# Kernel optimization log

Hardware: AMD Instinct MI355X
Metric: run time of the kernel (lower is better)

## Reference

```python
import jax, jax.numpy as jnp
from jax import lax
import numpy as np

B, S, D, H, L, DFF = 64, 512, 512, 8, 6, 2048
CLIP_C = 10.0
EPS = 1e-5


def setup_inputs() -> dict:
    key = jax.random.key(0)
    ks = jax.random.split(key, 16)
    sc = 0.02
    inp = {
        "x": jax.random.normal(ks[0], (B, S, D), jnp.float32),
        "mask": jnp.zeros((B, S, S), jnp.float32),
        # stacked per-layer params [L, ...]; Linear stored as (out, in) like torch
        "qkv_w": jax.random.normal(ks[1], (L, 3 * D, D), jnp.float32) * sc,
        "qkv_b": jnp.zeros((L, 3 * D), jnp.float32),
        "ln1_g": jnp.ones((L, D), jnp.float32),
        "ln1_b": jnp.zeros((L, D), jnp.float32),
        "kv_w": jax.random.normal(ks[2], (L, 2 * D, D), jnp.float32) * sc,
        "kv_b": jnp.zeros((L, 2 * D), jnp.float32),
        "ln2_g": jnp.ones((L, D), jnp.float32),
        "ln2_b": jnp.zeros((L, D), jnp.float32),
        "w1": jax.random.normal(ks[3], (L, DFF, D), jnp.float32) * sc,
        "b1": jnp.zeros((L, DFF), jnp.float32),
        "w2": jax.random.normal(ks[4], (L, D, DFF), jnp.float32) * sc,
        "b2": jnp.zeros((L, D), jnp.float32),
        "ln3_g": jnp.ones((L, D), jnp.float32),
        "ln3_b": jnp.zeros((L, D), jnp.float32),
    }
    return inp


def _ln(v, g, b):
    m = v.mean(-1, keepdims=True)
    var = ((v - m) ** 2).mean(-1, keepdims=True)
    return (v - m) * lax.rsqrt(var + EPS) * g + b


def _mha(q, k, v, mask, clip_c):
    # faithful to custom_multi_head_attn: bmm -> /sqrt(hd) -> [c*tanh] -> +mask -> softmax -> bmm
    b, sq, d = q.shape
    sk = k.shape[1]
    hd = d // H
    qh = q.reshape(b, sq, H, hd)
    kh = k.reshape(b, sk, H, hd)
    vh = v.reshape(b, sk, H, hd)
    s = jnp.einsum('bqhd,bkhd->bhqk', qh, kh) * (1.0 / float(hd) ** 0.5)
    if clip_c is not None:
        s = clip_c * jnp.tanh(s)
    if mask is not None:
        s = s + mask[:, None]  # repeat over heads
    a = jax.nn.softmax(s, axis=-1)
    return jnp.einsum('bhqk,bkhd->bqhd', a, vh).reshape(b, sq, d)


def reference(x, mask, qkv_w, qkv_b, ln1_g, ln1_b, kv_w, kv_b, ln2_g, ln2_b,
              w1, b1, w2, b2, ln3_g, ln3_b):
    def step(h, p):
        (qw, qb, g1, be1, kw, kb, g2, be2, fw1, fb1, fw2, fb2, g3, be3) = p
        # self-attention block (no FFN, no mask, no clip; note: NO out-projection,
        # matching the original which never applies out_proj_weight)
        qkv = h @ qw.T + qb
        q, k, v = jnp.split(qkv, 3, axis=-1)
        x1 = _ln(h + _mha(q, k, v, None, None), g1, be1)
        # cross-attention block: query = sa output (no q_proj), kv from original h
        kv_ = h @ kw.T + kb
        k2, v2 = jnp.split(kv_, 2, axis=-1)
        y = _ln(x1 + _mha(x1, k2, v2, mask, CLIP_C), g2, be2)
        # FFN + residual + norm (post-norm)
        ff = jax.nn.relu(y @ fw1.T + fb1) @ fw2.T + fb2
        return _ln(y + ff, g3, be3), None

    params = (qkv_w, qkv_b, ln1_g, ln1_b, kv_w, kv_b, ln2_g, ln2_b,
              w1, b1, w2, b2, ln3_g, ln3_b)
    out, _ = lax.scan(step, x, params)
    return out
```

## Files before the change

### kernel.cpp

```cpp
#include <hip/hip_runtime.h>


typedef __bf16 bf16_t;
typedef __bf16 bf16x8 __attribute__((ext_vector_type(8)));
typedef __bf16 bf16x4 __attribute__((ext_vector_type(4)));
typedef float  f32x4  __attribute__((ext_vector_type(4)));

#define NB   64
#define NS   512
#define ND   512
#define NH   8
#define NHD  64
#define NL   6
#define NDFF 2048
#define NM   (NB * NS)

__device__ __forceinline__ void gld_lds16(const void* gsrc, void* lds) {
  __builtin_amdgcn_global_load_lds((__attribute__((address_space(1))) void*)gsrc,
                                   (__attribute__((address_space(3))) void*)lds,
                                   16, 0, 0);
}

template<int N> __device__ __forceinline__ void vm_wait() {
  if constexpr (N == 0)      asm volatile("s_waitcnt vmcnt(0)" ::: "memory");
  else if constexpr (N == 3) asm volatile("s_waitcnt vmcnt(3)" ::: "memory");
}
__device__ __forceinline__ void lgkm0() {
  asm volatile("s_waitcnt lgkmcnt(0)" ::: "memory");
}

__global__ __launch_bounds__(256) void cvt_f32_bf16(const float* __restrict__ in,
                                                    bf16_t* __restrict__ out,
                                                    long n) {
  long i = ((long)blockIdx.x * 256 + threadIdx.x) * 8;
  const long stride = (long)gridDim.x * 256 * 8;
  for (; i < n; i += stride) {
    f32x4 a = *(const f32x4*)(in + i);
    f32x4 b = *(const f32x4*)(in + i + 4);
    bf16x8 o;
#pragma unroll
    for (int j = 0; j < 4; ++j) { o[j] = (bf16_t)a[j]; o[j + 4] = (bf16_t)b[j]; }
    *(bf16x8*)(out + i) = o;
  }
}

template<bool RELU, bool BIAS_ROW>
__global__ __launch_bounds__(512, 4) void gemm128n(const bf16_t* __restrict__ Ap,
                                                   const bf16_t* __restrict__ Wp,
                                                   const float* __restrict__ bias,
                                                   bf16_t* __restrict__ Cout,
                                                   int Nn, int Kk) {
  __shared__ __attribute__((aligned(16))) bf16_t As[2][256 * 32];
  __shared__ __attribute__((aligned(16))) bf16_t Bs[2][128 * 32];
  const int tid = threadIdx.x;
  const int l   = tid & 63;
  const int w   = tid >> 6;
  const int wr  = w >> 2;
  const int wc  = w & 3;
  const int l15 = l & 15, lg = l >> 4;

  const int nn   = Nn >> 7;
  const int nwg  = gridDim.x;
  const int flat = blockIdx.x;
  const int wgid = (nwg & 7) ? flat : (flat & 7) * (nwg >> 3) + (flat >> 3);
  const int m0 = (wgid / nn) * 256;
  const int n0 = (wgid % nn) * 128;

  const int srow = tid >> 2;
  const int sg   = (tid & 3) ^ (srow & 3);

  auto stA = [&](int bf_, int p, int kc) {
    gld_lds16(Ap + (size_t)(m0 + p * 128 + srow) * Kk + kc + sg * 8,
              &As[bf_][(p * 128 + w * 16) * 32]);
  };
  auto stB = [&](int bf_, int kc) {
    gld_lds16(Wp + (size_t)(n0 + srow) * Kk + kc + sg * 8,
              &Bs[bf_][(w * 16) * 32]);
  };
  auto stage = [&](int kt, int bf_) {
    const int kc = kt * 32;
    stA(bf_, 0, kc); stA(bf_, 1, kc); stB(bf_, kc);
  };
  auto ldA = [&](int bf_, int mi) -> bf16x8 {
    const int row = wr * 128 + mi * 16 + l15;
    return *(const bf16x8*)&As[bf_][row * 32 + ((lg ^ (row & 3)) * 8)];
  };
  auto ldB = [&](int bf_, int ni) -> bf16x8 {
    const int row = wc * 32 + ni * 16 + l15;
    return *(const bf16x8*)&Bs[bf_][row * 32 + ((lg ^ (row & 3)) * 8)];
  };

  f32x4 acc[8][2];
#pragma unroll
  for (int i = 0; i < 8; ++i) { acc[i][0] = (f32x4){0,0,0,0}; acc[i][1] = (f32x4){0,0,0,0}; }

  const int KT = Kk >> 5;
  stage(0, 0);
  stage(1, 1);

  for (int kt = 0; kt < KT; ++kt) {
    const int buf = kt & 1;
    if (kt + 1 < KT) vm_wait<3>(); else vm_wait<0>();
    __builtin_amdgcn_s_barrier();

    bf16x8 bf0 = ldB(buf, 0), bf1 = ldB(buf, 1);
    __builtin_amdgcn_s_setprio(1);
#pragma unroll
    for (int mi = 0; mi < 8; ++mi) {
      bf16x8 af = ldA(buf, mi);
      acc[mi][0] = __builtin_amdgcn_mfma_f32_16x16x32_bf16(af, bf0, acc[mi][0], 0, 0, 0);
      acc[mi][1] = __builtin_amdgcn_mfma_f32_16x16x32_bf16(af, bf1, acc[mi][1], 0, 0, 0);
    }
    __builtin_amdgcn_s_setprio(0);

    lgkm0();
    __builtin_amdgcn_s_barrier();
    if (kt + 2 < KT) stage(kt + 2, buf);
  }

#pragma unroll
  for (int mf = 0; mf < 8; ++mf)
#pragma unroll
    for (int ni = 0; ni < 2; ++ni) {
      const int col = n0 + wc * 32 + ni * 16 + l15;
      const float bc = BIAS_ROW ? 0.f : bias[col];
#pragma unroll
      for (int r = 0; r < 4; ++r) {
        const int rowi = m0 + wr * 128 + mf * 16 + lg * 4 + r;
        float v = acc[mf][ni][r] + (BIAS_ROW ? bias[rowi] : bc);
        if (RELU) v = fmaxf(v, 0.f);
        Cout[(size_t)rowi * Nn + col] = (bf16_t)v;
      }
    }
}

template<int CROSS>
__global__ __launch_bounds__(256, 2) void attn3(const bf16_t* __restrict__ Q,
                                                const bf16_t* __restrict__ K,
                                                const bf16_t* __restrict__ Vt,
                                                const float* __restrict__ maskp,
                                                bf16_t* __restrict__ O,
                                                int qstride, int kstride, int vstride) {
  __shared__ __attribute__((aligned(16))) bf16_t k_s[2][128 * 64];
  __shared__ __attribute__((aligned(16))) bf16_t v_s[2][64 * 128];
  __shared__ __attribute__((aligned(16))) bf16_t p_s[64 * 128];

  const int tid = threadIdx.x;
  const int l   = tid & 63;
  const int w   = tid >> 6;
  const int bid = blockIdx.x;
  const int h   = bid & 7;
  const int qt  = (bid >> 3) & 7;
  const int b   = bid >> 6;
  const int h64 = h * NHD;
  const int l15 = l & 15, lg = l >> 4;

  const int qglob = qt * 64 + w * 16 + l15;

  auto stageK = [&](int kt, int buf) {
#pragma unroll
    for (int i = 0; i < 4; ++i) {
      const int r  = (w * 4 + i) * 8 + (l >> 3);
      const int c8 = (l & 7) ^ (r & 7);
      gld_lds16(K + (size_t)(b * NS + kt * 128 + r) * kstride + h64 + c8 * 8,
                &k_s[buf][(w * 4 + i) * 512]);
    }
  };
  auto stageV = [&](int kt, int buf) {
#pragma unroll
    for (int i = 0; i < 4; ++i) {
      const int d = w * 16 + i * 4 + (l >> 4);
      const int g = (l & 15) ^ (d & 15);
      gld_lds16(Vt + (size_t)(h64 + d) * vstride + b * NS + kt * 128 + g * 8,
                &v_s[buf][(w * 16 + i * 4) * 128]);
    }
  };

  stageK(0, 0); stageV(0, 0);

  bf16x8 qf[2];
#pragma unroll
  for (int c = 0; c < 2; ++c)
    qf[c] = *(const bf16x8*)(Q + (size_t)(b * NS + qglob) * qstride + h64 + c * 32 + lg * 8);

  f32x4 mk[2][8];
  if (CROSS) {
#pragma unroll
    for (int nt = 0; nt < 8; ++nt)
      mk[0][nt] = *(const f32x4*)(maskp + (size_t)(b * NS + qglob) * NS + nt * 16 + lg * 4);
  }

  float m_run = -3e38f, l_run = 0.f;
  const f32x4 zz = {0.f, 0.f, 0.f, 0.f};
  f32x4 oacc[4] = {zz, zz, zz, zz};

#pragma unroll
  for (int kt = 0; kt < 4; ++kt) {
    const int buf = kt & 1;
    __syncthreads();
    if (kt < 3) {
      stageK(kt + 1, buf ^ 1);
      stageV(kt + 1, buf ^ 1);
      if (CROSS) {
#pragma unroll
        for (int nt = 0; nt < 8; ++nt)
          mk[(kt + 1) & 1][nt] = *(const f32x4*)(maskp + (size_t)(b * NS + qglob) * NS
                                                 + (kt + 1) * 128 + nt * 16 + lg * 4);
      }
    }

    f32x4 s[8];
    __builtin_amdgcn_s_setprio(1);
#pragma unroll
    for (int nt = 0; nt < 8; ++nt) {
      const int row = nt * 16 + l15;
      bf16x8 ka0 = *(const bf16x8*)((const char*)k_s[buf] + row * 128 + ((lg ^ (row & 7)) * 16));
      bf16x8 ka1 = *(const bf16x8*)((const char*)k_s[buf] + row * 128 + (((4 + lg) ^ (row & 7)) * 16));
      f32x4 z = zz;
      z = __builtin_amdgcn_mfma_f32_16x16x32_bf16(ka0, qf[0], z, 0, 0, 0);
      z = __builtin_amdgcn_mfma_f32_16x16x32_bf16(ka1, qf[1], z, 0, 0, 0);
      s[nt] = z;
    }
    __builtin_amdgcn_s_setprio(0);

    float tmax = -3e38f;
#pragma unroll
    for (int nt = 0; nt < 8; ++nt) {
      f32x4 v = s[nt] * 0.125f;
      if (CROSS) {
#pragma unroll
        for (int r = 0; r < 4; ++r) {
          const float e2 = __expf(2.f * v[r]);
          v[r] = 10.f - 20.f * __builtin_amdgcn_rcpf(e2 + 1.f) + mk[buf][nt][r];
        }
      }
      s[nt] = v;
#pragma unroll
      for (int r = 0; r < 4; ++r) tmax = fmaxf(tmax, v[r]);
    }
    tmax = fmaxf(tmax, __shfl_xor(tmax, 16, 64));
    tmax = fmaxf(tmax, __shfl_xor(tmax, 32, 64));
    const float m_new = fmaxf(m_run, tmax);
    const float f = __expf(m_run - m_new);
    float fq[4];
#pragma unroll
    for (int r = 0; r < 4; ++r) fq[r] = __shfl(f, lg * 4 + r, 64);
#pragma unroll
    for (int dt = 0; dt < 4; ++dt)
#pragma unroll
      for (int r = 0; r < 4; ++r) oacc[dt][r] *= fq[r];

    float ts = 0.f;
#pragma unroll
    for (int nt = 0; nt < 8; ++nt) {
      f32x4 v = s[nt];
#pragma unroll
      for (int r = 0; r < 4; ++r) { const float e = __expf(v[r] - m_new); ts += e; v[r] = e; }
      s[nt] = v;
    }
    l_run = l_run * f + ts;
    m_run = m_new;

    const int prow = w * 16 + l15;
#pragma unroll
    for (int nt = 0; nt < 8; ++nt) {
      bf16x4 pk;
#pragma unroll
      for (int r = 0; r < 4; ++r) pk[r] = (bf16_t)s[nt][r];
      const int gran = (nt * 2 + (lg >> 1)) ^ (prow & 15);
      *(bf16x4*)((char*)p_s + prow * 256 + gran * 16 + (lg & 1) * 8) = pk;
    }

    __builtin_amdgcn_s_setprio(1);
#pragma unroll
    for (int ks = 0; ks < 4; ++ks) {
      const int ag = (ks * 4 + lg) ^ (prow & 15);
      bf16x8 pa = *(const bf16x8*)((const char*)p_s + prow * 256 + ag * 16);
#pragma unroll
      for (int dt = 0; dt < 4; ++dt) {
        const int vrow = dt * 16 + l15;
        const int vg   = (ks * 4 + lg) ^ (vrow & 15);
        bf16x8 vb = *(const bf16x8*)((const char*)v_s[buf] + vrow * 256 + vg * 16);
        oacc[dt] = __builtin_amdgcn_mfma_f32_16x16x32_bf16(pa, vb, oacc[dt], 0, 0, 0);
      }
    }
    __builtin_amdgcn_s_setprio(0);
  }

  l_run += __shfl_xor(l_run, 16, 64);
  l_run += __shfl_xor(l_run, 32, 64);
  const float inv = 1.f / l_run;
  float invq[4];
#pragma unroll
  for (int r = 0; r < 4; ++r) invq[r] = __shfl(inv, lg * 4 + r, 64);
#pragma unroll
  for (int dt = 0; dt < 4; ++dt)
#pragma unroll
    for (int r = 0; r < 4; ++r) {
      const size_t row = (size_t)(b * NS + qt * 64 + w * 16 + lg * 4 + r);
      O[row * ND + h64 + dt * 16 + l15] = (bf16_t)(oacc[dt][r] * invq[r]);
    }
}

template<bool A16, bool W32>
__global__ __launch_bounds__(256) void add_ln2(const void* __restrict__ Xav,
                                               const bf16_t* __restrict__ Xb,
                                               const float* __restrict__ gw,
                                               const float* __restrict__ bw,
                                               float* __restrict__ o32,
                                               bf16_t* __restrict__ o16) {
  const int l = threadIdx.x & 63;
  const size_t row  = (size_t)blockIdx.x * 4 + (threadIdx.x >> 6);
  const size_t base = row * ND + l * 8;
  f32x4 a0, a1;
  if (A16) {
    bf16x8 t = *(const bf16x8*)((const bf16_t*)Xav + base);
#pragma unroll
    for (int i = 0; i < 4; ++i) { a0[i] = (float)t[i]; a1[i] = (float)t[i + 4]; }
  } else {
    a0 = *(const f32x4*)((const float*)Xav + base);
    a1 = *(const f32x4*)((const float*)Xav + base + 4);
  }
  bf16x8 tb = *(const bf16x8*)(Xb + base);
  f32x4 b0, b1;
#pragma unroll
  for (int i = 0; i < 4; ++i) { b0[i] = (float)tb[i]; b1[i] = (float)tb[i + 4]; }
  f32x4 v0 = a0 + b0, v1 = a1 + b1;
  float s = v0[0] + v0[1] + v0[2] + v0[3] + v1[0] + v1[1] + v1[2] + v1[3];
#pragma unroll
  for (int off = 1; off < 64; off <<= 1) s += __shfl_xor(s, off, 64);
  const float mean = s * (1.f / ND);
  f32x4 d0 = v0 - mean, d1 = v1 - mean;
  float q = d0[0]*d0[0] + d0[1]*d0[1] + d0[2]*d0[2] + d0[3]*d0[3]
          + d1[0]*d1[0] + d1[1]*d1[1] + d1[2]*d1[2] + d1[3]*d1[3];
#pragma unroll
  for (int off = 1; off < 64; off <<= 1) q += __shfl_xor(q, off, 64);
  const float rstd = rsqrtf(q * (1.f / ND) + 1e-5f);
  const f32x4 g0 = *(const f32x4*)(gw + l * 8), g1 = *(const f32x4*)(gw + l * 8 + 4);
  const f32x4 h0 = *(const f32x4*)(bw + l * 8), h1 = *(const f32x4*)(bw + l * 8 + 4);
  f32x4 r0 = d0 * rstd * g0 + h0;
  f32x4 r1 = d1 * rstd * g1 + h1;
  if (W32) {
    *(f32x4*)(o32 + base)     = r0;
    *(f32x4*)(o32 + base + 4) = r1;
  } else {
    bf16x8 o;
#pragma unroll
    for (int i = 0; i < 4; ++i) { o[i] = (bf16_t)r0[i]; o[i + 4] = (bf16_t)r1[i]; }
    *(bf16x8*)(o16 + base) = o;
  }
}

extern "C" void kernel_launch(void* const* d_in, const int* in_sizes, int n_in,
                              void* d_out, int out_size, void* d_ws, size_t ws_size,
                              hipStream_t stream) {
  (void)in_sizes; (void)n_in; (void)out_size;
  const float* x     = (const float*)d_in[0];
  const float* maskp = (const float*)d_in[1];
  const float* qkvw  = (const float*)d_in[2];
  const float* qkvb  = (const float*)d_in[3];
  const float* ln1g  = (const float*)d_in[4];
  const float* ln1b  = (const float*)d_in[5];
  const float* kvw   = (const float*)d_in[6];
  const float* kvb   = (const float*)d_in[7];
  const float* ln2g  = (const float*)d_in[8];
  const float* ln2b  = (const float*)d_in[9];
  const float* w1p   = (const float*)d_in[10];
  const float* b1p   = (const float*)d_in[11];
  const float* w2p   = (const float*)d_in[12];
  const float* b2p   = (const float*)d_in[13];
  const float* ln3g  = (const float*)d_in[14];
  const float* ln3b  = (const float*)d_in[15];
  float* out = (float*)d_out;

  const size_t WALL = 40894464, WLYR = 6815744, H16B = 33554432;
  struct Tier { int R; bool allw; };
  const Tier tiers[6] = {{32768, true}, {16384, true}, {8192, true},
                         {4096, true}, {2048, false}, {1024, false}};
  int R = 0; bool allw = false;
  for (int t = 0; t < 6; ++t) {
    size_t need = (tiers[t].allw ? WALL : WLYR) + H16B +
                  (size_t)tiers[t].R * 7168 + 16384;
    if (ws_size >= need) { R = tiers[t].R; allw = tiers[t].allw; break; }
  }
  if (R == 0) return;
  const int nchunks = NM / R;
  const int CB = R / NS;
  const int MT = R / 256;

  char* p = (char*)d_ws;
  auto alloc = [&](size_t bytes) { char* r = p; p += (bytes + 255) & ~(size_t)255; return r; };
  bf16_t* WQ = (bf16_t*)alloc((allw ? NL : 1) * (size_t)1536 * ND * 2);
  bf16_t* WK = (bf16_t*)alloc((allw ? NL : 1) * (size_t)1024 * ND * 2);
  bf16_t* W1 = (bf16_t*)alloc((allw ? NL : 1) * (size_t)NDFF * ND * 2);
  bf16_t* W2 = (bf16_t*)alloc((allw ? NL : 1) * (size_t)ND * NDFF * 2);
  bf16_t* h16  = (bf16_t*)alloc((size_t)NM * ND * 2);
  bf16_t* big  = (bf16_t*)alloc((size_t)R * NDFF * 2);
  bf16_t* t16  = (bf16_t*)alloc((size_t)R * ND * 2);
  bf16_t* x116 = (bf16_t*)alloc((size_t)R * ND * 2);
  bf16_t* y16  = (bf16_t*)alloc((size_t)R * ND * 2);

  auto cvt = [&](const float* src, bf16_t* dst, long n) {
    int blocks = (int)((n / 8 + 255) / 256); if (blocks > 8192) blocks = 8192;
    hipLaunchKernelGGL(cvt_f32_bf16, dim3(blocks), dim3(256), 0, stream, src, dst, n);
  };

  cvt(x, h16, (long)NM * ND);
  if (allw) {
    cvt(qkvw, WQ, (long)NL * 1536 * ND);
    cvt(kvw,  WK, (long)NL * 1024 * ND);
    cvt(w1p,  W1, (long)NL * NDFF * ND);
    cvt(w2p,  W2, (long)NL * ND * NDFF);
  }

  for (int l = 0; l < NL; ++l) {
    const bf16_t *wq_l, *wk_l, *w1_l, *w2_l;
    if (allw) {
      wq_l = WQ + (size_t)l * 1536 * ND;
      wk_l = WK + (size_t)l * 1024 * ND;
      w1_l = W1 + (size_t)l * NDFF * ND;
      w2_l = W2 + (size_t)l * ND * NDFF;
    } else {
      cvt(qkvw + (size_t)l * 1536 * ND, WQ, (long)1536 * ND);
      cvt(kvw  + (size_t)l * 1024 * ND, WK, (long)1024 * ND);
      cvt(w1p  + (size_t)l * NDFF * ND, W1, (long)NDFF * ND);
      cvt(w2p  + (size_t)l * ND * NDFF, W2, (long)ND * NDFF);
      wq_l = WQ; wk_l = WK; w1_l = W1; w2_l = W2;
    }

    for (int c = 0; c < nchunks; ++c) {
      const size_t r0 = (size_t)c * R;
      bf16_t*       h16c  = h16 + r0 * ND;
      const float*  maskc = maskp + r0 * NS;
      bf16_t* vtS = big + (size_t)R * 1024;
      bf16_t* vtC = big + (size_t)R * 512;

      hipLaunchKernelGGL(HIP_KERNEL_NAME(gemm128n<false, false>), dim3(MT * 8), dim3(512), 0, stream,
                         h16c, wq_l, qkvb + l * 1536, big, 1024, 512);
      hipLaunchKernelGGL(HIP_KERNEL_NAME(gemm128n<false, true>), dim3(2 * (R / 128)), dim3(512), 0, stream,
                         wq_l + (size_t)1024 * 512, h16c, qkvb + l * 1536 + 1024, vtS, R, 512);
      hipLaunchKernelGGL(HIP_KERNEL_NAME(attn3<0>), dim3(CB * 64), dim3(256), 0, stream,
                         big, big + 512, vtS, (const float*)nullptr, t16, 1024, 1024, R);
      if (l == 0)
        hipLaunchKernelGGL(HIP_KERNEL_NAME(add_ln2<false, false>), dim3(R / 4), dim3(256), 0, stream,
                           (const void*)(x + r0 * ND), t16, ln1g, ln1b, (float*)nullptr, x116);
      else
        hipLaunchKernelGGL(HIP_KERNEL_NAME(add_ln2<true, false>), dim3(R / 4), dim3(256), 0, stream,
                           (const void*)h16c, t16, ln1g + l * ND, ln1b + l * ND, (float*)nullptr, x116);
      hipLaunchKernelGGL(HIP_KERNEL_NAME(gemm128n<false, false>), dim3(MT * 4), dim3(512), 0, stream,
                         h16c, wk_l, kvb + l * 1024, big, 512, 512);
      hipLaunchKernelGGL(HIP_KERNEL_NAME(gemm128n<false, true>), dim3(2 * (R / 128)), dim3(512), 0, stream,
                         wk_l + (size_t)512 * 512, h16c, kvb + l * 1024 + 512, vtC, R, 512);
      hipLaunchKernelGGL(HIP_KERNEL_NAME(attn3<1>), dim3(CB * 64), dim3(256), 0, stream,
                         x116, big, vtC, maskc, t16, 512, 512, R);
      hipLaunchKernelGGL(HIP_KERNEL_NAME(add_ln2<true, false>), dim3(R / 4), dim3(256), 0, stream,
                         (const void*)x116, t16, ln2g + l * ND, ln2b + l * ND, (float*)nullptr, y16);
      hipLaunchKernelGGL(HIP_KERNEL_NAME(gemm128n<true, false>), dim3(MT * 16), dim3(512), 0, stream,
                         y16, w1_l, b1p + l * NDFF, big, 2048, 512);
      hipLaunchKernelGGL(HIP_KERNEL_NAME(gemm128n<false, false>), dim3(MT * 4), dim3(512), 0, stream,
                         big, w2_l, b2p + l * ND, t16, 512, 2048);
      if (l < NL - 1)
        hipLaunchKernelGGL(HIP_KERNEL_NAME(add_ln2<true, false>), dim3(R / 4), dim3(256), 0, stream,
                           (const void*)y16, t16, ln3g + l * ND, ln3b + l * ND, (float*)nullptr, h16c);
      else
        hipLaunchKernelGGL(HIP_KERNEL_NAME(add_ln2<true, true>), dim3(R / 4), dim3(256), 0, stream,
                           (const void*)y16, t16, ln3g + l * ND, ln3b + l * ND, out + r0 * ND, (bf16_t*)nullptr);
    }
  }
}
```

Measured before the change: 4.062 ms.

## Retile GEMM to 128x256 squarer warp tiles, shrink attention KV tile, add bf16 mask

The GEMM changes from 256x128 tiles with 8x2 MFMA fragments per warp to 128x256 tiles with 4x4 fragments per warp. This raises fragment reuse per LDS load and changes grid sizes. The attention kernel now uses 64-key tiles instead of 128, halving LDS use so it can run at occupancy 4 instead of 2. When workspace allows, the mask is converted once to bf16 to halve its read traffic in cross-attention, at the cost of an extra conversion pass and a larger workspace.

```diff
diff --git a/kernel.cpp b/kernel.cpp
--- a/kernel.cpp
+++ b/kernel.cpp
@@ -45,13 +45,13 @@
 }
 
 template<bool RELU, bool BIAS_ROW>
-__global__ __launch_bounds__(512, 4) void gemm128n(const bf16_t* __restrict__ Ap,
-                                                   const bf16_t* __restrict__ Wp,
-                                                   const float* __restrict__ bias,
-                                                   bf16_t* __restrict__ Cout,
-                                                   int Nn, int Kk) {
-  __shared__ __attribute__((aligned(16))) bf16_t As[2][256 * 32];
-  __shared__ __attribute__((aligned(16))) bf16_t Bs[2][128 * 32];
+__global__ __launch_bounds__(512, 4) void gemm64(const bf16_t* __restrict__ Ap,
+                                                 const bf16_t* __restrict__ Wp,
+                                                 const float* __restrict__ bias,
+                                                 bf16_t* __restrict__ Cout,
+                                                 int Nn, int Kk) {
+  __shared__ __attribute__((aligned(16))) bf16_t As[2][128 * 32];
+  __shared__ __attribute__((aligned(16))) bf16_t Bs[2][256 * 32];
   const int tid = threadIdx.x;
   const int l   = tid & 63;
   const int w   = tid >> 6;
@@ -59,40 +59,42 @@
   const int wc  = w & 3;
   const int l15 = l & 15, lg = l >> 4;
 
-  const int nn   = Nn >> 7;
+  const int nn   = Nn >> 8;
   const int nwg  = gridDim.x;
   const int flat = blockIdx.x;
   const int wgid = (nwg & 7) ? flat : (flat & 7) * (nwg >> 3) + (flat >> 3);
-  const int m0 = (wgid / nn) * 256;
-  const int n0 = (wgid % nn) * 128;
+  const int m0 = (wgid / nn) * 128;
+  const int n0 = (wgid % nn) * 256;
 
   const int srow = tid >> 2;
   const int sg   = (tid & 3) ^ (srow & 3);
 
-  auto stA = [&](int bf_, int p, int kc) {
-    gld_lds16(Ap + (size_t)(m0 + p * 128 + srow) * Kk + kc + sg * 8,
-              &As[bf_][(p * 128 + w * 16) * 32]);
-  };
-  auto stB = [&](int bf_, int kc) {
-    gld_lds16(Wp + (size_t)(n0 + srow) * Kk + kc + sg * 8,
-              &Bs[bf_][(w * 16) * 32]);
+  auto stA = [&](int bf_, int kc) {
+    gld_lds16(Ap + (size_t)(m0 + srow) * Kk + kc + sg * 8,
+              &As[bf_][(w * 16) * 32]);
+  };
+  auto stB = [&](int bf_, int p, int kc) {
+    gld_lds16(Wp + (size_t)(n0 + p * 128 + srow) * Kk + kc + sg * 8,
+              &Bs[bf_][(p * 128 + w * 16) * 32]);
   };
   auto stage = [&](int kt, int bf_) {
     const int kc = kt * 32;
-    stA(bf_, 0, kc); stA(bf_, 1, kc); stB(bf_, kc);
+    stA(bf_, kc); stB(bf_, 0, kc); stB(bf_, 1, kc);
   };
   auto ldA = [&](int bf_, int mi) -> bf16x8 {
-    const int row = wr * 128 + mi * 16 + l15;
+    const int row = wr * 64 + mi * 16 + l15;
     return *(const bf16x8*)&As[bf_][row * 32 + ((lg ^ (row & 3)) * 8)];
   };
   auto ldB = [&](int bf_, int ni) -> bf16x8 {
-    const int row = wc * 32 + ni * 16 + l15;
+    const int row = wc * 64 + ni * 16 + l15;
     return *(const bf16x8*)&Bs[bf_][row * 32 + ((lg ^ (row & 3)) * 8)];
   };
 
-  f32x4 acc[8][2];
-#pragma unroll
-  for (int i = 0; i < 8; ++i) { acc[i][0] = (f32x4){0,0,0,0}; acc[i][1] = (f32x4){0,0,0,0}; }
+  f32x4 acc[4][4];
+#pragma unroll
+  for (int i = 0; i < 4; ++i)
+#pragma unroll
+    for (int j = 0; j < 4; ++j) acc[i][j] = (f32x4){0.f, 0.f, 0.f, 0.f};
 
   const int KT = Kk >> 5;
   stage(0, 0);
@@ -103,14 +105,15 @@
     if (kt + 1 < KT) vm_wait<3>(); else vm_wait<0>();
     __builtin_amdgcn_s_barrier();
 
-    bf16x8 bf0 = ldB(buf, 0), bf1 = ldB(buf, 1);
+    bf16x8 af[4], bfr[4];
+#pragma unroll
+    for (int i = 0; i < 4; ++i) { af[i] = ldA(buf, i); bfr[i] = ldB(buf, i); }
     __builtin_amdgcn_s_setprio(1);
 #pragma unroll
-    for (int mi = 0; mi < 8; ++mi) {
-      bf16x8 af = ldA(buf, mi);
-      acc[mi][0] = __builtin_amdgcn_mfma_f32_16x16x32_bf16(af, bf0, acc[mi][0], 0, 0, 0);
-      acc[mi][1] = __builtin_amdgcn_mfma_f32_16x16x32_bf16(af, bf1, acc[mi][1], 0, 0, 0);
-    }
+    for (int mi = 0; mi < 4; ++mi)
+#pragma unroll
+      for (int ni = 0; ni < 4; ++ni)
+        acc[mi][ni] = __builtin_amdgcn_mfma_f32_16x16x32_bf16(af[mi], bfr[ni], acc[mi][ni], 0, 0, 0);
     __builtin_amdgcn_s_setprio(0);
 
     lgkm0();
@@ -119,31 +122,31 @@
   }
 
 #pragma unroll
-  for (int mf = 0; mf < 8; ++mf)
-#pragma unroll
-    for (int ni = 0; ni < 2; ++ni) {
-      const int col = n0 + wc * 32 + ni * 16 + l15;
+  for (int mi = 0; mi < 4; ++mi)
+#pragma unroll
+    for (int ni = 0; ni < 4; ++ni) {
+      const int col = n0 + wc * 64 + ni * 16 + l15;
       const float bc = BIAS_ROW ? 0.f : bias[col];
 #pragma unroll
       for (int r = 0; r < 4; ++r) {
-        const int rowi = m0 + wr * 128 + mf * 16 + lg * 4 + r;
-        float v = acc[mf][ni][r] + (BIAS_ROW ? bias[rowi] : bc);
+        const int rowi = m0 + wr * 64 + mi * 16 + lg * 4 + r;
+        float v = acc[mi][ni][r] + (BIAS_ROW ? bias[rowi] : bc);
         if (RELU) v = fmaxf(v, 0.f);
         Cout[(size_t)rowi * Nn + col] = (bf16_t)v;
       }
     }
 }
 
-template<int CROSS>
-__global__ __launch_bounds__(256, 2) void attn3(const bf16_t* __restrict__ Q,
+template<int CROSS, bool M16>
+__global__ __launch_bounds__(256, 4) void attn5(const bf16_t* __restrict__ Q,
                                                 const bf16_t* __restrict__ K,
                                                 const bf16_t* __restrict__ Vt,
-                                                const float* __restrict__ maskp,
+                                                const void* __restrict__ maskp,
                                                 bf16_t* __restrict__ O,
                                                 int qstride, int kstride, int vstride) {
-  __shared__ __attribute__((aligned(16))) bf16_t k_s[2][128 * 64];
-  __shared__ __attribute__((aligned(16))) bf16_t v_s[2][64 * 128];
-  __shared__ __attribute__((aligned(16))) bf16_t p_s[64 * 128];
+  __shared__ __attribute__((aligned(16))) bf16_t k_s[2][64 * 64];
+  __shared__ __attribute__((aligned(16))) bf16_t v_s[2][64 * 64];
+  __shared__ __attribute__((aligned(16))) bf16_t p_s[64 * 64];
 
   const int tid = threadIdx.x;
   const int l   = tid & 63;
@@ -159,20 +162,20 @@
 
   auto stageK = [&](int kt, int buf) {
 #pragma unroll
-    for (int i = 0; i < 4; ++i) {
-      const int r  = (w * 4 + i) * 8 + (l >> 3);
-      const int c8 = (l & 7) ^ (r & 7);
-      gld_lds16(K + (size_t)(b * NS + kt * 128 + r) * kstride + h64 + c8 * 8,
-                &k_s[buf][(w * 4 + i) * 512]);
+    for (int i = 0; i < 2; ++i) {
+      const int r  = i * 32 + (tid >> 3);
+      const int c8 = (tid & 7) ^ (r & 7);
+      gld_lds16(K + (size_t)(b * NS + kt * 64 + r) * kstride + h64 + c8 * 8,
+                &k_s[buf][(i * 32 + w * 8) * 64]);
     }
   };
   auto stageV = [&](int kt, int buf) {
 #pragma unroll
-    for (int i = 0; i < 4; ++i) {
-      const int d = w * 16 + i * 4 + (l >> 4);
-      const int g = (l & 15) ^ (d & 15);
-      gld_lds16(Vt + (size_t)(h64 + d) * vstride + b * NS + kt * 128 + g * 8,
-                &v_s[buf][(w * 16 + i * 4) * 128]);
+    for (int i = 0; i < 2; ++i) {
+      const int d = i * 32 + (tid >> 3);
+      const int g = (tid & 7) ^ (d & 7);
+      gld_lds16(Vt + (size_t)(h64 + d) * vstride + b * NS + kt * 64 + g * 8,
+                &v_s[buf][(i * 32 + w * 8) * 64]);
     }
   };
 
@@ -183,11 +186,16 @@
   for (int c = 0; c < 2; ++c)
     qf[c] = *(const bf16x8*)(Q + (size_t)(b * NS + qglob) * qstride + h64 + c * 32 + lg * 8);
 
-  f32x4 mk[2][8];
+  bf16x4 mk16[2][4];
+  f32x4  mkf[2][4];
   if (CROSS) {
 #pragma unroll
-    for (int nt = 0; nt < 8; ++nt)
-      mk[0][nt] = *(const f32x4*)(maskp + (size_t)(b * NS + qglob) * NS + nt * 16 + lg * 4);
+    for (int nt = 0; nt < 4; ++nt) {
+      if (M16) mk16[0][nt] = *(const bf16x4*)((const bf16_t*)maskp
+                              + (size_t)(b * NS + qglob) * NS + nt * 16 + lg * 4);
+      else     mkf[0][nt]  = *(const f32x4*)((const float*)maskp
+                              + (size_t)(b * NS + qglob) * NS + nt * 16 + lg * 4);
+    }
   }
 
   float m_run = -3e38f, l_run = 0.f;
@@ -195,24 +203,27 @@
   f32x4 oacc[4] = {zz, zz, zz, zz};
 
 #pragma unroll
-  for (int kt = 0; kt < 4; ++kt) {
+  for (int kt = 0; kt < 8; ++kt) {
     const int buf = kt & 1;
     __syncthreads();
-    if (kt < 3) {
+    if (kt < 7) {
       stageK(kt + 1, buf ^ 1);
       stageV(kt + 1, buf ^ 1);
       if (CROSS) {
 #pragma unroll
-        for (int nt = 0; nt < 8; ++nt)
-          mk[(kt + 1) & 1][nt] = *(const f32x4*)(maskp + (size_t)(b * NS + qglob) * NS
-                                                 + (kt + 1) * 128 + nt * 16 + lg * 4);
+        for (int nt = 0; nt < 4; ++nt) {
+          if (M16) mk16[buf ^ 1][nt] = *(const bf16x4*)((const bf16_t*)maskp
+                     + (size_t)(b * NS + qglob) * NS + (kt + 1) * 64 + nt * 16 + lg * 4);
+          else     mkf[buf ^ 1][nt]  = *(const f32x4*)((const float*)maskp
+                     + (size_t)(b * NS + qglob) * NS + (kt + 1) * 64 + nt * 16 + lg * 4);
+        }
       }
     }
 
-    f32x4 s[8];
+    f32x4 s[4];
     __builtin_amdgcn_s_setprio(1);
 #pragma unroll
-    for (int nt = 0; nt < 8; ++nt) {
+    for (int nt = 0; nt < 4; ++nt) {
       const int row = nt * 16 + l15;
       bf16x8 ka0 = *(const bf16x8*)((const char*)k_s[buf] + row * 128 + ((lg ^ (row & 7)) * 16));
       bf16x8 ka1 = *(const bf16x8*)((const char*)k_s[buf] + row * 128 + (((4 + lg) ^ (row & 7)) * 16));
@@ -225,13 +236,14 @@
 
     float tmax = -3e38f;
 #pragma unroll
-    for (int nt = 0; nt < 8; ++nt) {
+    for (int nt = 0; nt < 4; ++nt) {
       f32x4 v = s[nt] * 0.125f;
       if (CROSS) {
 #pragma unroll
         for (int r = 0; r < 4; ++r) {
           const float e2 = __expf(2.f * v[r]);
-          v[r] = 10.f - 20.f * __builtin_amdgcn_rcpf(e2 + 1.f) + mk[buf][nt][r];
+          const float mkv = M16 ? (float)mk16[buf][nt][r] : mkf[buf][nt][r];
+          v[r] = 10.f - 20.f * __builtin_amdgcn_rcpf(e2 + 1.f) + mkv;
         }
       }
       s[nt] = v;
@@ -252,7 +264,7 @@
 
     float ts = 0.f;
 #pragma unroll
-    for (int nt = 0; nt < 8; ++nt) {
+    for (int nt = 0; nt < 4; ++nt) {
       f32x4 v = s[nt];
 #pragma unroll
       for (int r = 0; r < 4; ++r) { const float e = __expf(v[r] - m_new); ts += e; v[r] = e; }
@@ -263,24 +275,24 @@
 
     const int prow = w * 16 + l15;
 #pragma unroll
-    for (int nt = 0; nt < 8; ++nt) {
+    for (int nt = 0; nt < 4; ++nt) {
       bf16x4 pk;
 #pragma unroll
       for (int r = 0; r < 4; ++r) pk[r] = (bf16_t)s[nt][r];
-      const int gran = (nt * 2 + (lg >> 1)) ^ (prow & 15);
-      *(bf16x4*)((char*)p_s + prow * 256 + gran * 16 + (lg & 1) * 8) = pk;
+      const int gran = (nt * 2 + (lg >> 1)) ^ (prow & 7);
+      *(bf16x4*)((char*)p_s + prow * 128 + gran * 16 + (lg & 1) * 8) = pk;
     }
 
     __builtin_amdgcn_s_setprio(1);
 #pragma unroll
-    for (int ks = 0; ks < 4; ++ks) {
-      const int ag = (ks * 4 + lg) ^ (prow & 15);
-      bf16x8 pa = *(const bf16x8*)((const char*)p_s + prow * 256 + ag * 16);
+    for (int ks = 0; ks < 2; ++ks) {
+      const int ag = (ks * 4 + lg) ^ (prow & 7);
+      bf16x8 pa = *(const bf16x8*)((const char*)p_s + prow * 128 + ag * 16);
 #pragma unroll
       for (int dt = 0; dt < 4; ++dt) {
         const int vrow = dt * 16 + l15;
-        const int vg   = (ks * 4 + lg) ^ (vrow & 15);
-        bf16x8 vb = *(const bf16x8*)((const char*)v_s[buf] + vrow * 256 + vg * 16);
+        const int vg   = (ks * 4 + lg) ^ (vrow & 7);
+        bf16x8 vb = *(const bf16x8*)((const char*)v_s[buf] + vrow * 128 + vg * 16);
         oacc[dt] = __builtin_amdgcn_mfma_f32_16x16x32_bf16(pa, vb, oacc[dt], 0, 0, 0);
       }
     }
@@ -373,20 +385,21 @@
   const float* ln3b  = (const float*)d_in[15];
   float* out = (float*)d_out;
 
-  const size_t WALL = 40894464, WLYR = 6815744, H16B = 33554432;
+  const size_t WALL = 40894464, WLYR = 6815744, H16B = 33554432, M16B = 33554432;
   struct Tier { int R; bool allw; };
   const Tier tiers[6] = {{32768, true}, {16384, true}, {8192, true},
                          {4096, true}, {2048, false}, {1024, false}};
-  int R = 0; bool allw = false;
+  int R = 0; bool allw = false; size_t base_need = 0;
   for (int t = 0; t < 6; ++t) {
     size_t need = (tiers[t].allw ? WALL : WLYR) + H16B +
                   (size_t)tiers[t].R * 7168 + 16384;
-    if (ws_size >= need) { R = tiers[t].R; allw = tiers[t].allw; break; }
+    if (ws_size >= need) { R = tiers[t].R; allw = tiers[t].allw; base_need = need; break; }
   }
   if (R == 0) return;
+  const bool m16 = (ws_size >= base_need + M16B + 256);
   const int nchunks = NM / R;
   const int CB = R / NS;
-  const int MT = R / 256;
+  const int MT = R / 128;
 
   char* p = (char*)d_ws;
   auto alloc = [&](size_t bytes) { char* r = p; p += (bytes + 255) & ~(size_t)255; return r; };
@@ -399,6 +412,7 @@
   bf16_t* t16  = (bf16_t*)alloc((size_t)R * ND * 2);
   bf16_t* x116 = (bf16_t*)alloc((size_t)R * ND * 2);
   bf16_t* y16  = (bf16_t*)alloc((size_t)R * ND * 2);
+  bf16_t* mask16 = m16 ? (bf16_t*)alloc(M16B) : nullptr;
 
   auto cvt = [&](const float* src, bf16_t* dst, long n) {
     int blocks = (int)((n / 8 + 255) / 256); if (blocks > 8192) blocks = 8192;
@@ -406,6 +420,7 @@
   };
 
   cvt(x, h16, (long)NM * ND);
+  if (m16) cvt(maskp, mask16, (long)NM * NS);
   if (allw) {
     cvt(qkvw, WQ, (long)NL * 1536 * ND);
     cvt(kvw,  WK, (long)NL * 1024 * ND);
@@ -431,33 +446,36 @@
     for (int c = 0; c < nchunks; ++c) {
       const size_t r0 = (size_t)c * R;
       bf16_t*       h16c  = h16 + r0 * ND;
-      const float*  maskc = maskp + r0 * NS;
       bf16_t* vtS = big + (size_t)R * 1024;
       bf16_t* vtC = big + (size_t)R * 512;
 
-      hipLaunchKernelGGL(HIP_KERNEL_NAME(gemm128n<false, false>), dim3(MT * 8), dim3(512), 0, stream,
+      hipLaunchKernelGGL(HIP_KERNEL_NAME(gemm64<false, false>), dim3(MT * 4), dim3(512), 0, stream,
                          h16c, wq_l, qkvb + l * 1536, big, 1024, 512);
-      hipLaunchKernelGGL(HIP_KERNEL_NAME(gemm128n<false, true>), dim3(2 * (R / 128)), dim3(512), 0, stream,
+      hipLaunchKernelGGL(HIP_KERNEL_NAME(gemm64<false, true>), dim3(4 * (R / 256)), dim3(512), 0, stream,
                          wq_l + (size_t)1024 * 512, h16c, qkvb + l * 1536 + 1024, vtS, R, 512);
-      hipLaunchKernelGGL(HIP_KERNEL_NAME(attn3<0>), dim3(CB * 64), dim3(256), 0, stream,
-                         big, big + 512, vtS, (const float*)nullptr, t16, 1024, 1024, R);
+      hipLaunchKernelGGL(HIP_KERNEL_NAME(attn5<0, false>), dim3(CB * 64), dim3(256), 0, stream,
+                         big, big + 512, vtS, (const void*)nullptr, t16, 1024, 1024, R);
       if (l == 0)
         hipLaunchKernelGGL(HIP_KERNEL_NAME(add_ln2<false, false>), dim3(R / 4), dim3(256), 0, stream,
                            (const void*)(x + r0 * ND), t16, ln1g, ln1b, (float*)nullptr, x116);
       else
         hipLaunchKernelGGL(HIP_KERNEL_NAME(add_ln2<true, false>), dim3(R / 4), dim3(256), 0, stream,
                            (const void*)h16c, t16, ln1g + l * ND, ln1b + l * ND, (float*)nullptr, x116);
-      hipLaunchKernelGGL(HIP_KERNEL_NAME(gemm128n<false, false>), dim3(MT * 4), dim3(512), 0, stream,
+      hipLaunchKernelGGL(HIP_KERNEL_NAME(gemm64<false, false>), dim3(MT * 2), dim3(512), 0, stream,
                          h16c, wk_l, kvb + l * 1024, big, 512, 512);
-      hipLaunchKernelGGL(HIP_KERNEL_NAME(gemm128n<false, true>), dim3(2 * (R / 128)), dim3(512), 0, stream,
+      hipLaunchKernelGGL(HIP_KERNEL_NAME(gemm64<false, true>), dim3(4 * (R / 256)), dim3(512), 0, stream,
                          wk_l + (size_t)512 * 512, h16c, kvb + l * 1024 + 512, vtC, R, 512);
-      hipLaunchKernelGGL(HIP_KERNEL_NAME(attn3<1>), dim3(CB * 64), dim3(256), 0, stream,
-                         x116, big, vtC, maskc, t16, 512, 512, R);
+      if (m16)
+        hipLaunchKernelGGL(HIP_KERNEL_NAME(attn5<1, true>), dim3(CB * 64), dim3(256), 0, stream,
+                           x116, big, vtC, (const void*)(mask16 + r0 * NS), t16, 512, 512, R);
+      else
+        hipLaunchKernelGGL(HIP_KERNEL_NAME(attn5<1, false>), dim3(CB * 64), dim3(256), 0, stream,
+                           x116, big, vtC, (const void*)(maskp + r0 * NS), t16, 512, 512, R);
       hipLaunchKernelGGL(HIP_KERNEL_NAME(add_ln2<true, false>), dim3(R / 4), dim3(256), 0, stream,
                          (const void*)x116, t16, ln2g + l * ND, ln2b + l * ND, (float*)nullptr, y16);
-      hipLaunchKernelGGL(HIP_KERNEL_NAME(gemm128n<true, false>), dim3(MT * 16), dim3(512), 0, stream,
+      hipLaunchKernelGGL(HIP_KERNEL_NAME(gemm64<true, false>), dim3(MT * 8), dim3(512), 0, stream,
                          y16, w1_l, b1p + l * NDFF, big, 2048, 512);
-      hipLaunchKernelGGL(HIP_KERNEL_NAME(gemm128n<false, false>), dim3(MT * 4), dim3(512), 0, stream,
+      hipLaunchKernelGGL(HIP_KERNEL_NAME(gemm64<false, false>), dim3(MT * 2), dim3(512), 0, stream,
                          big, w2_l, b2p + l * ND, t16, 512, 2048);
       if (l < NL - 1)
         hipLaunchKernelGGL(HIP_KERNEL_NAME(add_ln2<true, false>), dim3(R / 4), dim3(256), 0, stream,
```

Result: slower. 5.095 ms (+25.4%).
